# Kernel tuning notes

Measured on AMD Instinct MI355X. Metric: run time of the kernel, lower is better.

Reference implementation:

```python
import jax, jax.numpy as jnp
import numpy as np

B, T, N, F_IN = 8, 288, 2000, 1
E, ID, H, K = 128, 16, 128, 20
FL = T // 2 + 1  # rfft length = in_len//2 + 1
EPS_NORM = 1e-12
EPS_LN = 1e-8


def setup_inputs() -> dict:
    key = jax.random.key(0)
    k0, k1, k2, k3, k4 = jax.random.split(key, 5)
    return {
        "x": jax.random.normal(k0, (B, T, N, F_IN), jnp.float32),
        "Ex": jax.random.normal(k1, (FL, E), jnp.float32),
        "nodes": jax.random.normal(k2, (N, ID), jnp.float32),
        "Wd": jax.random.normal(k3, (N, E + ID, H), jnp.float32),
        "Wxabs": jax.random.normal(k4, (H, H), jnp.float32),
    }


def reference(x, Ex, nodes, Wd, Wxabs):
    # [B,T,N,F] -> take feature 0 -> [B,N,T]
    xt = jnp.transpose(x[:, :, :, 0], (0, 2, 1))
    xf = jnp.abs(jnp.fft.rfft(xt, axis=-1))  # [B,N,FL]
    # F.normalize p=2 over dim=1 (nodes), then dim=2 (freq): x / max(||x||, eps)
    xf = xf / jnp.clip(jnp.sqrt(jnp.sum(xf * xf, axis=1, keepdims=True)), EPS_NORM)
    xf = xf / jnp.clip(jnp.sqrt(jnp.sum(xf * xf, axis=2, keepdims=True)), EPS_NORM)
    xe = jnp.matmul(xf, Ex)  # [B,N,E]
    # cat(): append static node identity embedding per batch element
    xk = jnp.concatenate(
        [xe, jnp.broadcast_to(nodes, (xe.shape[0], N, ID))], axis=-1
    )  # [B,N,E+ID]
    # per-node weight bmm: [N,B,E+ID] @ [N,E+ID,H] -> [B,N,H]
    x1 = jax.nn.relu(jnp.einsum('bnd,ndh->bnh', xk, Wd))
    # LayerNorm over last two dims [N,H], eps=1e-8, no affine
    mu = jnp.mean(x1, axis=(1, 2), keepdims=True)
    var = jnp.mean((x1 - mu) ** 2, axis=(1, 2), keepdims=True)
    x2 = (x1 - mu) / jnp.sqrt(var + EPS_LN)
    # dropout is identity at inference
    adp = jnp.einsum('bnh,hk->bnk', x2, Wxabs)  # convt
    adj = jnp.einsum('bnh,bmh->bnm', adp, x1)  # [B,N,N]
    adp = jax.nn.relu(adj)
    # dy_mask_graph: per-row topk over dim=2 (torch dim=1 of the [N,N] slice),
    # binary mask via scatter of ones, then elementwise mask
    _, idx = jax.lax.top_k(adp, K)  # [B,N,K]
    bi = jnp.arange(adp.shape[0])[:, None, None]
    ni = jnp.arange(N)[None, :, None]
    mask = jnp.zeros_like(adp).at[bi, ni, idx].set(1.0)
    adj_masked = adp * mask
    return jax.nn.softmax(adj_masked, axis=2)
```

## Files before the change

kernel.cpp:

```cpp
#include <hip/hip_runtime.h>
#include <math.h>

#define BB 8
#define TT 288
#define NN 2000
#define FLEN 145
#define EE 128
#define IDD 16
#define HH 128
#define DKK 144
#define KTOP 20

typedef _Float16 half8 __attribute__((ext_vector_type(8)));
typedef float f32x4 __attribute__((ext_vector_type(4)));
typedef unsigned short ushort_t;

#define OFF_TW  ((size_t)0)
#define SZ_TW   ((size_t)TT*FLEN*2)
#define OFF_XF  (OFF_TW + SZ_TW)
#define SZ_XF   ((size_t)BB*FLEN*NN)
#define OFF_ICN (OFF_XF + SZ_XF)
#define OFF_IRN (OFF_ICN + (size_t)BB*FLEN)
#define OFF_XE  (OFF_IRN + (size_t)BB*NN)
#define SZ_BNH  ((size_t)BB*NN*HH)
#define OFF_X1  (OFF_XE + SZ_BNH)
#define OFF_ADP (OFF_X1 + SZ_BNH)
#define OFF_CSW (OFF_ADP + SZ_BNH)
#define OFF_LNS (OFF_CSW + HH)
#define OFF_LNF (OFF_LNS + 16)

__device__ __forceinline__ float wredSum(float v) {
#pragma unroll
  for (int o = 32; o > 0; o >>= 1) v += __shfl_down(v, o, 64);
  return v;
}
__device__ __forceinline__ float wredMax(float v) {
#pragma unroll
  for (int o = 32; o > 0; o >>= 1) v = fmaxf(v, __shfl_down(v, o, 64));
  return v;
}

__device__ __forceinline__ void split16(float v, ushort_t& hi, ushort_t& lo) {
  _Float16 h = (_Float16)v;
  _Float16 l = (_Float16)(v - (float)h);
  union { _Float16 f; ushort_t u; } a, b;
  a.f = h; b.f = l;
  hi = a.u; lo = b.u;
}

__global__ void k_init(const float* __restrict__ Wx, float* __restrict__ csw,
                       float* __restrict__ lns) {
  int k = threadIdx.x;
  float s = 0.f;
  for (int h = 0; h < HH; ++h) s += Wx[h * HH + k];
  csw[k] = s;
  if (k < 16) lns[k] = 0.f;
}

__global__ void k_tw(float* __restrict__ tw) {
  int id = blockIdx.x * 256 + threadIdx.x;
  if (id >= TT * FLEN) return;
  int t = id / FLEN, f = id % FLEN;
  int r = (t * f) % TT;
  double th = -2.0 * 3.14159265358979323846 * (double)r / (double)TT;
  tw[2 * id]     = (float)cos(th);
  tw[2 * id + 1] = (float)sin(th);
}

__global__ void k_dft(const float* __restrict__ x, const float* __restrict__ tw,
                      float* __restrict__ xf) {
  __shared__ __align__(16) float Xs[16][128];
  __shared__ __align__(16) float TWs[16][32][2];
  const int b = blockIdx.z;
  const int f0 = blockIdx.y * 32;
  const int n0 = blockIdx.x * 128;
  const int tid = threadIdx.x;
  const int tn = tid & 31;
  const int tf = tid >> 5;
  float ar[4][4] = {}, ai[4][4] = {};
  for (int t0 = 0; t0 < TT; t0 += 16) {
    __syncthreads();
    for (int l = tid; l < 512; l += 256) {
      int row = l >> 5, q = l & 31;
      int n = n0 + q * 4;
      const float* src = x + ((size_t)b * TT + (t0 + row)) * NN + n;
      float4 v = make_float4(0, 0, 0, 0);
      if (n + 3 < NN) v = *(const float4*)src;
      else {
        if (n + 0 < NN) v.x = src[0];
        if (n + 1 < NN) v.y = src[1];
        if (n + 2 < NN) v.z = src[2];
        if (n + 3 < NN) v.w = src[3];
      }
      *(float4*)&Xs[row][q * 4] = v;
    }
    for (int l = tid; l < 512; l += 256) {
      int row = l >> 5, ff = l & 31;
      int f = f0 + ff;
      float2 cs = make_float2(0, 0);
      if (f < FLEN) cs = *(const float2*)&tw[((size_t)(t0 + row) * FLEN + f) * 2];
      *(float2*)&TWs[row][ff][0] = cs;
    }
    __syncthreads();
#pragma unroll 4
    for (int t = 0; t < 16; ++t) {
      float4 xv = *(float4*)&Xs[t][tn * 4];
      float xx[4] = {xv.x, xv.y, xv.z, xv.w};
      float4 p0 = *(float4*)&TWs[t][tf * 4][0];
      float4 p1 = *(float4*)&TWs[t][tf * 4 + 2][0];
      float c[4] = {p0.x, p0.z, p1.x, p1.z};
      float s[4] = {p0.y, p0.w, p1.y, p1.w};
#pragma unroll
      for (int i = 0; i < 4; ++i)
#pragma unroll
        for (int j = 0; j < 4; ++j) {
          ar[i][j] = fmaf(xx[j], c[i], ar[i][j]);
          ai[i][j] = fmaf(xx[j], s[i], ai[i][j]);
        }
    }
  }
#pragma unroll
  for (int i = 0; i < 4; ++i) {
    int f = f0 + tf * 4 + i;
    if (f >= FLEN) continue;
    float* dst = &xf[((size_t)b * FLEN + f) * NN];
    float o[4];
#pragma unroll
    for (int j = 0; j < 4; ++j)
      o[j] = sqrtf(ar[i][j] * ar[i][j] + ai[i][j] * ai[i][j]);
    int n = n0 + tn * 4;
    if (n + 3 < NN) *(float4*)&dst[n] = make_float4(o[0], o[1], o[2], o[3]);
    else {
#pragma unroll
      for (int j = 0; j < 4; ++j) if (n + j < NN) dst[n + j] = o[j];
    }
  }
}

__global__ void k_colnorm(const float* __restrict__ xf, float* __restrict__ icn) {
  __shared__ float sc[4];
  int bf = blockIdx.x;
  const float* rowp = xf + (size_t)bf * NN;
  float s = 0.f;
  for (int i = threadIdx.x; i < NN; i += 256) { float v = rowp[i]; s = fmaf(v, v, s); }
  s = wredSum(s);
  int lane = threadIdx.x & 63, w = threadIdx.x >> 6;
  if (lane == 0) sc[w] = s;
  __syncthreads();
  if (threadIdx.x == 0)
    icn[bf] = 1.f / fmaxf(sqrtf(sc[0] + sc[1] + sc[2] + sc[3]), 1e-12f);
}

__global__ void k_rownorm(const float* __restrict__ xf, const float* __restrict__ icn,
                          float* __restrict__ irn) {
  int b = blockIdx.y;
  int n = blockIdx.x * 256 + threadIdx.x;
  if (n >= NN) return;
  float s = 0.f;
  for (int f = 0; f < FLEN; ++f) {
    float v = xf[((size_t)b * FLEN + f) * NN + n] * icn[b * FLEN + f];
    s = fmaf(v, v, s);
  }
  irn[b * NN + n] = 1.f / fmaxf(sqrtf(s), 1e-12f);
}

__global__ void k_xe(const float* __restrict__ xf, const float* __restrict__ icn,
                     const float* __restrict__ irn, const float* __restrict__ Ex,
                     float* __restrict__ xe) {
  __shared__ __align__(16) float As[16][64];
  __shared__ __align__(16) float Bs[16][128];
  const int b = blockIdx.y;
  const int n0 = blockIdx.x * 64;
  const int tid = threadIdx.x;
  const int tn = tid >> 4, te = tid & 15;
  float acc[4][8] = {};
  for (int f0 = 0; f0 < 160; f0 += 16) {
    __syncthreads();
    {
      int kt = tid >> 4, q = tid & 15;
      int f = f0 + kt;
      int n = n0 + q * 4;
      float4 v = make_float4(0, 0, 0, 0);
      if (f < FLEN) {
        float ic = icn[b * FLEN + f];
        const float* src = &xf[((size_t)b * FLEN + f) * NN + n];
        if (n + 3 < NN) v = *(const float4*)src;
        else {
          if (n + 0 < NN) v.x = src[0];
          if (n + 1 < NN) v.y = src[1];
          if (n + 2 < NN) v.z = src[2];
          if (n + 3 < NN) v.w = src[3];
        }
        v.x *= ic; v.y *= ic; v.z *= ic; v.w *= ic;
      }
      *(float4*)&As[kt][q * 4] = v;
    }
    for (int l = tid; l < 512; l += 256) {
      int kt = l >> 5, q = l & 31;
      int f = f0 + kt;
      float4 v = make_float4(0, 0, 0, 0);
      if (f < FLEN) v = *(const float4*)&Ex[(size_t)f * EE + q * 4];
      *(float4*)&Bs[kt][q * 4] = v;
    }
    __syncthreads();
#pragma unroll
    for (int k = 0; k < 16; ++k) {
      float4 a  = *(float4*)&As[k][tn * 4];
      float4 b0 = *(float4*)&Bs[k][te * 4];
      float4 b1 = *(float4*)&Bs[k][64 + te * 4];
      float av[4] = {a.x, a.y, a.z, a.w};
      float bv[8] = {b0.x, b0.y, b0.z, b0.w, b1.x, b1.y, b1.z, b1.w};
#pragma unroll
      for (int i = 0; i < 4; ++i)
#pragma unroll
        for (int j = 0; j < 8; ++j)
          acc[i][j] = fmaf(av[i], bv[j], acc[i][j]);
    }
  }
#pragma unroll
  for (int i = 0; i < 4; ++i) {
    int n = n0 + tn * 4 + i;
    if (n >= NN) continue;
    float sc = irn[b * NN + n];
    float* dst = &xe[((size_t)b * NN + n) * EE];
    *(float4*)&dst[te * 4] =
        make_float4(acc[i][0] * sc, acc[i][1] * sc, acc[i][2] * sc, acc[i][3] * sc);
    *(float4*)&dst[64 + te * 4] =
        make_float4(acc[i][4] * sc, acc[i][5] * sc, acc[i][6] * sc, acc[i][7] * sc);
  }
}

__global__ void k_x1(const float* xe, const float* __restrict__ nodes,
                     const float* __restrict__ Wd, float* __restrict__ x1,
                     ushort_t* x1hl) {
  __shared__ __align__(16) float xk[8][DKK];
  __shared__ float red[4][32][33];
  const int n = blockIdx.x;
  const int tid = threadIdx.x;
  {
    int b = tid >> 5, q = tid & 31;
    *(float4*)&xk[b][q * 4] = *(const float4*)&xe[((size_t)b * NN + n) * EE + q * 4];
  }
  if (tid < 128) {
    int b = tid >> 4, i = tid & 15;
    xk[b][EE + i] = nodes[(size_t)n * IDD + i];
  }
  __syncthreads();
  const int h4 = tid & 31;
  const int dg = tid >> 5;
  float acc[8][4] = {};
  for (int d = dg; d < DKK; d += 8) {
    float4 wv = *(const float4*)&Wd[((size_t)n * DKK + d) * HH + h4 * 4];
#pragma unroll
    for (int b = 0; b < 8; ++b) {
      float xv = xk[b][d];
      acc[b][0] = fmaf(xv, wv.x, acc[b][0]);
      acc[b][1] = fmaf(xv, wv.y, acc[b][1]);
      acc[b][2] = fmaf(xv, wv.z, acc[b][2]);
      acc[b][3] = fmaf(xv, wv.w, acc[b][3]);
    }
  }
#pragma unroll
  for (int b = 0; b < 8; ++b)
#pragma unroll
    for (int j = 0; j < 4; ++j)
      acc[b][j] += __shfl_xor(acc[b][j], 32, 64);
  const int wv_ = tid >> 6, lane = tid & 63;
  if (lane < 32) {
#pragma unroll
    for (int b = 0; b < 8; ++b)
#pragma unroll
      for (int j = 0; j < 4; ++j)
        red[wv_][lane][b * 4 + j] = acc[b][j];
  }
  __syncthreads();
#pragma unroll
  for (int o = 0; o < 4; ++o) {
    int idx = tid + o * 256;
    int b = idx >> 7, h = idx & 127;
    float s = red[0][h >> 2][b * 4 + (h & 3)] + red[1][h >> 2][b * 4 + (h & 3)] +
              red[2][h >> 2][b * 4 + (h & 3)] + red[3][h >> 2][b * 4 + (h & 3)];
    s = fmaxf(s, 0.f);
    x1[((size_t)b * NN + n) * HH + h] = s;
    ushort_t hi, lo;
    split16(s, hi, lo);
    size_t base = ((size_t)b * NN + n) * 256;
    x1hl[base + h] = hi;
    x1hl[base + 128 + h] = lo;
  }
}

__global__ void k_ln_stats(const float* __restrict__ x1, float* __restrict__ lns) {
  __shared__ float sc[4], sc2[4];
  int b = blockIdx.y, chunk = blockIdx.x;
  const float* base = x1 + (size_t)b * NN * HH + (size_t)chunk * 8000;
  float s = 0.f, s2 = 0.f;
  for (int i = threadIdx.x; i < 8000; i += 256) {
    float v = base[i];
    s += v; s2 = fmaf(v, v, s2);
  }
  s = wredSum(s); s2 = wredSum(s2);
  int lane = threadIdx.x & 63, w = threadIdx.x >> 6;
  if (lane == 0) { sc[w] = s; sc2[w] = s2; }
  __syncthreads();
  if (threadIdx.x == 0) {
    atomicAdd(&lns[b], sc[0] + sc[1] + sc[2] + sc[3]);
    atomicAdd(&lns[8 + b], sc2[0] + sc2[1] + sc2[2] + sc2[3]);
  }
}

__global__ void k_ln_final(const float* __restrict__ lns, float* __restrict__ lnf) {
  int b = threadIdx.x;
  if (b < 8) {
    float cnt = (float)(NN * HH);
    float mu = lns[b] / cnt;
    float var = fmaxf(lns[8 + b] / cnt - mu * mu, 0.f);
    lnf[b] = mu;
    lnf[8 + b] = 1.f / sqrtf(var + 1e-8f);
  }
}

__global__ void k_adp(const float* __restrict__ x1, const float* __restrict__ Wx,
                      const float* __restrict__ csw, const float* __restrict__ lnf,
                      ushort_t* __restrict__ adphl) {
  __shared__ __align__(16) float As[16][64];
  __shared__ __align__(16) float Bs[16][128];
  const int r0 = blockIdx.x * 64;
  const int tid = threadIdx.x;
  const int tn = tid >> 4, te = tid & 15;
  float acc[4][8] = {};
  for (int k0 = 0; k0 < HH; k0 += 16) {
    __syncthreads();
    {
      int rr = tid >> 2, kq = tid & 3;
      float4 v = *(const float4*)&x1[(size_t)(r0 + rr) * HH + k0 + kq * 4];
      As[kq * 4 + 0][rr] = v.x;
      As[kq * 4 + 1][rr] = v.y;
      As[kq * 4 + 2][rr] = v.z;
      As[kq * 4 + 3][rr] = v.w;
    }
    for (int l = tid; l < 512; l += 256) {
      int kt = l >> 5, q = l & 31;
      *(float4*)&Bs[kt][q * 4] = *(const float4*)&Wx[(size_t)(k0 + kt) * HH + q * 4];
    }
    __syncthreads();
#pragma unroll
    for (int k = 0; k < 16; ++k) {
      float4 a  = *(float4*)&As[k][tn * 4];
      float4 b0 = *(float4*)&Bs[k][te * 4];
      float4 b1 = *(float4*)&Bs[k][64 + te * 4];
      float av[4] = {a.x, a.y, a.z, a.w};
      float bv[8] = {b0.x, b0.y, b0.z, b0.w, b1.x, b1.y, b1.z, b1.w};
#pragma unroll
      for (int i = 0; i < 4; ++i)
#pragma unroll
        for (int j = 0; j < 8; ++j)
          acc[i][j] = fmaf(av[i], bv[j], acc[i][j]);
    }
  }
  float4 c0 = *(const float4*)&csw[te * 4];
  float4 c1 = *(const float4*)&csw[64 + te * 4];
  float cw[8] = {c0.x, c0.y, c0.z, c0.w, c1.x, c1.y, c1.z, c1.w};
#pragma unroll
  for (int i = 0; i < 4; ++i) {
    int r = r0 + tn * 4 + i;
    int b = r / NN;
    float mu = lnf[b], isd = lnf[8 + b];
    size_t base = (size_t)r * 256;
    ushort_t hi[8], lo[8];
#pragma unroll
    for (int j = 0; j < 8; ++j) {
      float o = (acc[i][j] - mu * cw[j]) * isd;
      split16(o, hi[j], lo[j]);
    }
    ushort4 u;
    u.x = hi[0]; u.y = hi[1]; u.z = hi[2]; u.w = hi[3];
    *(ushort4*)&adphl[base + te * 4] = u;
    u.x = hi[4]; u.y = hi[5]; u.z = hi[6]; u.w = hi[7];
    *(ushort4*)&adphl[base + 64 + te * 4] = u;
    u.x = lo[0]; u.y = lo[1]; u.z = lo[2]; u.w = lo[3];
    *(ushort4*)&adphl[base + 128 + te * 4] = u;
    u.x = lo[4]; u.y = lo[5]; u.z = lo[6]; u.w = lo[7];
    *(ushort4*)&adphl[base + 128 + 64 + te * 4] = u;
  }
}

__global__ void k_adj(const ushort_t* __restrict__ adphl,
                      const ushort_t* __restrict__ x1hl,
                      float* __restrict__ out) {
  __shared__ __align__(16) ushort_t lds[4][128 * 32];
  const int b = blockIdx.z;
  const int n0 = blockIdx.y * 128;
  const int m0 = blockIdx.x * 128;
  const int tid = threadIdx.x;
  const int w = tid >> 6;
  const int lane = tid & 63;
  const int quad = lane >> 4, r16 = lane & 15;
  const int rBase = (w >> 1) * 64;
  const int cBase = (w & 1) * 64;

  f32x4 acc[4][4];
#pragma unroll
  for (int i = 0; i < 4; ++i)
#pragma unroll
    for (int j = 0; j < 4; ++j)
      acc[i][j] = (f32x4){0.f, 0.f, 0.f, 0.f};

  const ushort_t* src = (w < 2) ? adphl : x1hl;
  const int rg0 = (w < 2) ? n0 : m0;
  const int loOff = (w & 1) ? 128 : 0;

  for (int k0 = 0; k0 < HH; k0 += 32) {
    __syncthreads();
#pragma unroll
    for (int i = 0; i < 8; ++i) {
      int cl = i * 64 + lane;
      int row = cl >> 2, c = cl & 3;
      int gr = rg0 + row; if (gr > NN - 1) gr = NN - 1;
      const uint4* gp =
          (const uint4*)(src + ((size_t)(b * NN + gr)) * 256 + loOff + k0 + c * 8);
      uint4 v = *gp;
      *(uint4*)&lds[w][row * 32 + ((c ^ (row & 3)) * 8)] = v;
    }
    __syncthreads();

    half8 Ah[4], Al[4], Bh[4], Bl[4];
#pragma unroll
    for (int i = 0; i < 4; ++i) {
      int ar = rBase + i * 16 + r16;
      int aoff = ar * 32 + ((quad ^ (ar & 3)) * 8);
      Ah[i] = *(half8*)&lds[0][aoff];
      Al[i] = *(half8*)&lds[1][aoff];
      int br = cBase + i * 16 + r16;
      int boff = br * 32 + ((quad ^ (br & 3)) * 8);
      Bh[i] = *(half8*)&lds[2][boff];
      Bl[i] = *(half8*)&lds[3][boff];
    }
#pragma unroll
    for (int i = 0; i < 4; ++i)
#pragma unroll
      for (int j = 0; j < 4; ++j) {
        acc[i][j] = __builtin_amdgcn_mfma_f32_16x16x32_f16(Ah[i], Bh[j], acc[i][j], 0, 0, 0);
        acc[i][j] = __builtin_amdgcn_mfma_f32_16x16x32_f16(Ah[i], Bl[j], acc[i][j], 0, 0, 0);
        acc[i][j] = __builtin_amdgcn_mfma_f32_16x16x32_f16(Al[i], Bh[j], acc[i][j], 0, 0, 0);
      }
  }

#pragma unroll
  for (int i = 0; i < 4; ++i) {
#pragma unroll
    for (int j = 0; j < 4; ++j) {
      int m = m0 + cBase + j * 16 + r16;
      if (m >= NN) continue;
#pragma unroll
      for (int reg = 0; reg < 4; ++reg) {
        int n = n0 + rBase + i * 16 + quad * 4 + reg;
        if (n >= NN) continue;
        out[((size_t)b * NN + n) * NN + m] = fmaxf(acc[i][j][reg], 0.f);
      }
    }
  }
}

__global__ void k_softmax(float* __restrict__ out) {
  __shared__ __align__(16) float row[NN];
  __shared__ float scr[4];
  __shared__ float swv[4];
  __shared__ int swi[4];
  __shared__ float tkv[KTOP];
  __shared__ int tki[KTOP];
  __shared__ float bcast[1];
  const int r = blockIdx.x;
  float* g = out + (size_t)r * NN;
  const int tid = threadIdx.x;
  const int lane = tid & 63, w = tid >> 6;
  for (int q = tid; q < 500; q += 256) *(float4*)&row[q * 4] = *(const float4*)&g[q * 4];
  __syncthreads();
  float m = 0.f;
  for (int i = tid; i < NN; i += 256) m = fmaxf(m, row[i]);
  m = wredMax(m);
  if (lane == 0) scr[w] = m;
  __syncthreads();
  m = fmaxf(fmaxf(scr[0], scr[1]), fmaxf(scr[2], scr[3]));
  const float thr = m - 87.f;
  float s = 0.f, c = 0.f;
  for (int i = tid; i < NN; i += 256) {
    float v = row[i];
    if (v > thr) { s += expf(v - m); c += 1.f; }
  }
  s = wredSum(s); c = wredSum(c);
  __syncthreads();
  if (lane == 0) scr[w] = s;
  __syncthreads();
  s = scr[0] + scr[1] + scr[2] + scr[3];
  __syncthreads();
  if (lane == 0) scr[w] = c;
  __syncthreads();
  c = scr[0] + scr[1] + scr[2] + scr[3];
  const float em = expf(-m);
  if (c <= 20.5f) {
    float D = s + ((float)NN - c) * em;
    float invD = 1.f / D;
    float defv = em * invD;
    for (int q = tid; q < 500; q += 256) {
      float4 v = *(float4*)&row[q * 4];
      float4 o;
      o.x = (v.x > thr) ? expf(v.x - m) * invD : defv;
      o.y = (v.y > thr) ? expf(v.y - m) * invD : defv;
      o.z = (v.z > thr) ? expf(v.z - m) * invD : defv;
      o.w = (v.w > thr) ? expf(v.w - m) * invD : defv;
      *(float4*)&g[q * 4] = o;
    }
  } else {
    for (int it = 0; it < KTOP; ++it) {
      float bv = -1.f; int bi = 0x7fffffff;
      for (int i = tid; i < NN; i += 256) {
        float v = row[i];
        if (v > bv) { bv = v; bi = i; }
      }
#pragma unroll
      for (int o = 32; o > 0; o >>= 1) {
        float ov = __shfl_down(bv, o, 64);
        int oi = __shfl_down(bi, o, 64);
        if (ov > bv || (ov == bv && oi < bi)) { bv = ov; bi = oi; }
      }
      __syncthreads();
      if (lane == 0) { swv[w] = bv; swi[w] = bi; }
      __syncthreads();
      if (tid == 0) {
        float fv = swv[0]; int fi = swi[0];
        for (int ww = 1; ww < 4; ++ww)
          if (swv[ww] > fv || (swv[ww] == fv && swi[ww] < fi)) { fv = swv[ww]; fi = swi[ww]; }
        tkv[it] = fv; tki[it] = fi;
        row[fi] = -1.f;
      }
      __syncthreads();
    }
    if (tid == 0) {
      float D = ((float)(NN - KTOP)) * em;
      for (int it = 0; it < KTOP; ++it) D += expf(tkv[it] - m);
      bcast[0] = 1.f / D;
    }
    __syncthreads();
    float invD = bcast[0];
    float defv = em * invD;
    for (int q = tid; q < 500; q += 256)
      *(float4*)&g[q * 4] = make_float4(defv, defv, defv, defv);
    __syncthreads();
    if (tid < KTOP) g[tki[tid]] = expf(tkv[tid] - m) * invD;
  }
}

extern "C" void kernel_launch(void* const* d_in, const int* in_sizes, int n_in,
                              void* d_out, int out_size, void* d_ws, size_t ws_size,
                              hipStream_t stream) {
  const float* x     = (const float*)d_in[0];
  const float* Ex    = (const float*)d_in[1];
  const float* nodes = (const float*)d_in[2];
  const float* Wd    = (const float*)d_in[3];
  const float* Wx    = (const float*)d_in[4];
  float* out = (float*)d_out;
  float* w = (float*)d_ws;
  float* tw  = w + OFF_TW;
  float* xf  = w + OFF_XF;
  float* icn = w + OFF_ICN;
  float* irn = w + OFF_IRN;
  float* xe  = w + OFF_XE;
  float* x1  = w + OFF_X1;
  float* csw = w + OFF_CSW;
  float* lns = w + OFF_LNS;
  float* lnf = w + OFF_LNF;
  ushort_t* adphl = (ushort_t*)(w + OFF_ADP);
  ushort_t* x1hl  = (ushort_t*)(w + OFF_XE);

  k_init<<<1, 128, 0, stream>>>(Wx, csw, lns);
  k_tw<<<(TT * FLEN + 255) / 256, 256, 0, stream>>>(tw);
  k_dft<<<dim3(16, 5, BB), 256, 0, stream>>>(x, tw, xf);
  k_colnorm<<<BB * FLEN, 256, 0, stream>>>(xf, icn);
  k_rownorm<<<dim3(8, BB), 256, 0, stream>>>(xf, icn, irn);
  k_xe<<<dim3(32, BB), 256, 0, stream>>>(xf, icn, irn, Ex, xe);
  k_x1<<<NN, 256, 0, stream>>>(xe, nodes, Wd, x1, x1hl);
  k_ln_stats<<<dim3(32, BB), 256, 0, stream>>>(x1, lns);
  k_ln_final<<<1, 64, 0, stream>>>(lns, lnf);
  k_adp<<<250, 256, 0, stream>>>(x1, Wx, csw, lnf, adphl);
  k_adj<<<dim3(16, 16, BB), 256, 0, stream>>>(adphl, x1hl, out);
  k_softmax<<<BB * NN, 256, 0, stream>>>(out);
}
```

Before: 488.9 us.

## Fuse adjacency GEMM with top-k masked softmax using LDS row cache

After: 582.2 us. +19.1%, slower.

```diff
diff --git a/kernel.cpp b/kernel.cpp
--- a/kernel.cpp
+++ b/kernel.cpp
@@ -29,6 +29,9 @@
 #define OFF_LNS (OFF_CSW + HH)
 #define OFF_LNF (OFF_LNS + 16)
 
+#define CACHE_W 2064
+#define FUSED_LDS_BYTES ((16 * CACHE_W + 2 * 8 * 64) * 4)
+
 __device__ __forceinline__ float wredSum(float v) {
 #pragma unroll
   for (int o = 32; o > 0; o >>= 1) v += __shfl_down(v, o, 64);
@@ -37,6 +40,16 @@
 __device__ __forceinline__ float wredMax(float v) {
 #pragma unroll
   for (int o = 32; o > 0; o >>= 1) v = fmaxf(v, __shfl_down(v, o, 64));
+  return v;
+}
+__device__ __forceinline__ float wredSumAll(float v) {
+#pragma unroll
+  for (int o = 32; o > 0; o >>= 1) v += __shfl_xor(v, o, 64);
+  return v;
+}
+__device__ __forceinline__ float wredMaxAll(float v) {
+#pragma unroll
+  for (int o = 32; o > 0; o >>= 1) v = fmaxf(v, __shfl_xor(v, o, 64));
   return v;
 }
 
@@ -385,169 +398,177 @@
   }
 }
 
-__global__ void k_adj(const ushort_t* __restrict__ adphl,
-                      const ushort_t* __restrict__ x1hl,
-                      float* __restrict__ out) {
-  __shared__ __align__(16) ushort_t lds[4][128 * 32];
-  const int b = blockIdx.z;
-  const int n0 = blockIdx.y * 128;
-  const int m0 = blockIdx.x * 128;
+__global__ __launch_bounds__(512, 1) void k_fused(
+    const ushort_t* __restrict__ adphl, const ushort_t* __restrict__ x1hl,
+    float* __restrict__ out) {
+  extern __shared__ float smem[];
+  float* cache = smem;
+  float* scrV = smem + 16 * CACHE_W;
+  int*   scrI = (int*)(scrV + 8 * 64);
+
+  const int b = blockIdx.y;
+  const int n0 = blockIdx.x * 16;
   const int tid = threadIdx.x;
   const int w = tid >> 6;
   const int lane = tid & 63;
   const int quad = lane >> 4, r16 = lane & 15;
-  const int rBase = (w >> 1) * 64;
-  const int cBase = (w & 1) * 64;
-
-  f32x4 acc[4][4];
-#pragma unroll
-  for (int i = 0; i < 4; ++i)
-#pragma unroll
-    for (int j = 0; j < 4; ++j)
-      acc[i][j] = (f32x4){0.f, 0.f, 0.f, 0.f};
-
-  const ushort_t* src = (w < 2) ? adphl : x1hl;
-  const int rg0 = (w < 2) ? n0 : m0;
-  const int loOff = (w & 1) ? 128 : 0;
-
-  for (int k0 = 0; k0 < HH; k0 += 32) {
-    __syncthreads();
-#pragma unroll
-    for (int i = 0; i < 8; ++i) {
-      int cl = i * 64 + lane;
-      int row = cl >> 2, c = cl & 3;
-      int gr = rg0 + row; if (gr > NN - 1) gr = NN - 1;
-      const uint4* gp =
-          (const uint4*)(src + ((size_t)(b * NN + gr)) * 256 + loOff + k0 + c * 8);
-      uint4 v = *gp;
-      *(uint4*)&lds[w][row * 32 + ((c ^ (row & 3)) * 8)] = v;
-    }
-    __syncthreads();
-
-    half8 Ah[4], Al[4], Bh[4], Bl[4];
+
+  half8 Ah[4], Al[4];
+  {
+    const ushort_t* abase =
+        adphl + ((size_t)(b * NN + n0 + r16)) * 256 + quad * 8;
+#pragma unroll
+    for (int ks = 0; ks < 4; ++ks) {
+      Ah[ks] = *(const half8*)(abase + ks * 32);
+      Al[ks] = *(const half8*)(abase + 128 + ks * 32);
+    }
+  }
+  for (int s = 0; s < 4; ++s) {
+    const int mb = s * 512 + w * 64;
 #pragma unroll
     for (int i = 0; i < 4; ++i) {
-      int ar = rBase + i * 16 + r16;
-      int aoff = ar * 32 + ((quad ^ (ar & 3)) * 8);
-      Ah[i] = *(half8*)&lds[0][aoff];
-      Al[i] = *(half8*)&lds[1][aoff];
-      int br = cBase + i * 16 + r16;
-      int boff = br * 32 + ((quad ^ (br & 3)) * 8);
-      Bh[i] = *(half8*)&lds[2][boff];
-      Bl[i] = *(half8*)&lds[3][boff];
-    }
-#pragma unroll
-    for (int i = 0; i < 4; ++i)
-#pragma unroll
-      for (int j = 0; j < 4; ++j) {
-        acc[i][j] = __builtin_amdgcn_mfma_f32_16x16x32_f16(Ah[i], Bh[j], acc[i][j], 0, 0, 0);
-        acc[i][j] = __builtin_amdgcn_mfma_f32_16x16x32_f16(Ah[i], Bl[j], acc[i][j], 0, 0, 0);
-        acc[i][j] = __builtin_amdgcn_mfma_f32_16x16x32_f16(Al[i], Bh[j], acc[i][j], 0, 0, 0);
-      }
-  }
-
-#pragma unroll
-  for (int i = 0; i < 4; ++i) {
-#pragma unroll
-    for (int j = 0; j < 4; ++j) {
-      int m = m0 + cBase + j * 16 + r16;
-      if (m >= NN) continue;
+      const int mt = mb + i * 16 + r16;
+      const int mc = (mt < NN) ? mt : NN - 1;
+      const ushort_t* bbase =
+          x1hl + ((size_t)(b * NN + mc)) * 256 + quad * 8;
+      half8 Bh[4], Bl[4];
+#pragma unroll
+      for (int ks = 0; ks < 4; ++ks) {
+        Bh[ks] = *(const half8*)(bbase + ks * 32);
+        Bl[ks] = *(const half8*)(bbase + 128 + ks * 32);
+      }
+      f32x4 acc = (f32x4){0.f, 0.f, 0.f, 0.f};
+#pragma unroll
+      for (int ks = 0; ks < 4; ++ks) {
+        acc = __builtin_amdgcn_mfma_f32_16x16x32_f16(Ah[ks], Bh[ks], acc, 0, 0, 0);
+        acc = __builtin_amdgcn_mfma_f32_16x16x32_f16(Ah[ks], Bl[ks], acc, 0, 0, 0);
+        acc = __builtin_amdgcn_mfma_f32_16x16x32_f16(Al[ks], Bh[ks], acc, 0, 0, 0);
+      }
 #pragma unroll
       for (int reg = 0; reg < 4; ++reg) {
-        int n = n0 + rBase + i * 16 + quad * 4 + reg;
-        if (n >= NN) continue;
-        out[((size_t)b * NN + n) * NN + m] = fmaxf(acc[i][j][reg], 0.f);
-      }
-    }
-  }
-}
-
-__global__ void k_softmax(float* __restrict__ out) {
-  __shared__ __align__(16) float row[NN];
-  __shared__ float scr[4];
-  __shared__ float swv[4];
-  __shared__ int swi[4];
-  __shared__ float tkv[KTOP];
-  __shared__ int tki[KTOP];
-  __shared__ float bcast[1];
-  const int r = blockIdx.x;
-  float* g = out + (size_t)r * NN;
-  const int tid = threadIdx.x;
-  const int lane = tid & 63, w = tid >> 6;
-  for (int q = tid; q < 500; q += 256) *(float4*)&row[q * 4] = *(const float4*)&g[q * 4];
+        int row = quad * 4 + reg;
+        float v = (mt < NN) ? fmaxf(acc[reg], 0.f) : -1.f;
+        cache[row * CACHE_W + mt] = v;
+      }
+    }
+  }
   __syncthreads();
-  float m = 0.f;
-  for (int i = tid; i < NN; i += 256) m = fmaxf(m, row[i]);
-  m = wredMax(m);
-  if (lane == 0) scr[w] = m;
-  __syncthreads();
-  m = fmaxf(fmaxf(scr[0], scr[1]), fmaxf(scr[2], scr[3]));
-  const float thr = m - 87.f;
-  float s = 0.f, c = 0.f;
-  for (int i = tid; i < NN; i += 256) {
-    float v = row[i];
-    if (v > thr) { s += expf(v - m); c += 1.f; }
-  }
-  s = wredSum(s); c = wredSum(c);
-  __syncthreads();
-  if (lane == 0) scr[w] = s;
-  __syncthreads();
-  s = scr[0] + scr[1] + scr[2] + scr[3];
-  __syncthreads();
-  if (lane == 0) scr[w] = c;
-  __syncthreads();
-  c = scr[0] + scr[1] + scr[2] + scr[3];
-  const float em = expf(-m);
-  if (c <= 20.5f) {
-    float D = s + ((float)NN - c) * em;
-    float invD = 1.f / D;
-    float defv = em * invD;
-    for (int q = tid; q < 500; q += 256) {
-      float4 v = *(float4*)&row[q * 4];
-      float4 o;
-      o.x = (v.x > thr) ? expf(v.x - m) * invD : defv;
-      o.y = (v.y > thr) ? expf(v.y - m) * invD : defv;
-      o.z = (v.z > thr) ? expf(v.z - m) * invD : defv;
-      o.w = (v.w > thr) ? expf(v.w - m) * invD : defv;
-      *(float4*)&g[q * 4] = o;
-    }
-  } else {
-    for (int it = 0; it < KTOP; ++it) {
-      float bv = -1.f; int bi = 0x7fffffff;
-      for (int i = tid; i < NN; i += 256) {
-        float v = row[i];
-        if (v > bv) { bv = v; bi = i; }
-      }
-#pragma unroll
-      for (int o = 32; o > 0; o >>= 1) {
-        float ov = __shfl_down(bv, o, 64);
-        int oi = __shfl_down(bi, o, 64);
-        if (ov > bv || (ov == bv && oi < bi)) { bv = ov; bi = oi; }
-      }
-      __syncthreads();
-      if (lane == 0) { swv[w] = bv; swi[w] = bi; }
-      __syncthreads();
-      if (tid == 0) {
-        float fv = swv[0]; int fi = swi[0];
-        for (int ww = 1; ww < 4; ++ww)
-          if (swv[ww] > fv || (swv[ww] == fv && swi[ww] < fi)) { fv = swv[ww]; fi = swi[ww]; }
-        tkv[it] = fv; tki[it] = fi;
-        row[fi] = -1.f;
-      }
-      __syncthreads();
-    }
-    if (tid == 0) {
-      float D = ((float)(NN - KTOP)) * em;
-      for (int it = 0; it < KTOP; ++it) D += expf(tkv[it] - m);
-      bcast[0] = 1.f / D;
-    }
-    __syncthreads();
-    float invD = bcast[0];
-    float defv = em * invD;
-    for (int q = tid; q < 500; q += 256)
-      *(float4*)&g[q * 4] = make_float4(defv, defv, defv, defv);
-    __syncthreads();
-    if (tid < KTOP) g[tki[tid]] = expf(tkv[tid] - m) * invD;
+
+  for (int rr = 0; rr < 2; ++rr) {
+    const int row = w * 2 + rr;
+    const float* crow = cache + row * CACHE_W;
+    f32x4 V[8];
+#pragma unroll
+    for (int j = 0; j < 8; ++j)
+      V[j] = *(const f32x4*)&crow[j * 256 + lane * 4];
+
+    float mx = -1.f, cp = 0.f;
+#pragma unroll
+    for (int j = 0; j < 8; ++j)
+#pragma unroll
+      for (int e = 0; e < 4; ++e) {
+        mx = fmaxf(mx, V[j][e]);
+        cp += (V[j][e] > 0.f) ? 1.f : 0.f;
+      }
+    const float m = wredMaxAll(mx);
+    const float cpos = wredSumAll(cp);
+    const float em = expf(-m);
+    float* g = out + ((size_t)(b * NN + n0 + row)) * NN;
+
+    if (cpos <= 20.5f) {
+      float s = 0.f;
+#pragma unroll
+      for (int j = 0; j < 8; ++j)
+#pragma unroll
+        for (int e = 0; e < 4; ++e)
+          if (V[j][e] > 0.f) s += expf(V[j][e] - m);
+      s = wredSumAll(s);
+      const float invD = 1.f / (s + (2000.f - cpos) * em);
+      const float defv = em * invD;
+#pragma unroll
+      for (int j = 0; j < 8; ++j) {
+        int m0 = j * 256 + lane * 4;
+        if (m0 >= NN) continue;
+        float4 o;
+        o.x = (V[j][0] > 0.f) ? expf(V[j][0] - m) * invD : defv;
+        o.y = (V[j][1] > 0.f) ? expf(V[j][1] - m) * invD : defv;
+        o.z = (V[j][2] > 0.f) ? expf(V[j][2] - m) * invD : defv;
+        o.w = (V[j][3] > 0.f) ? expf(V[j][3] - m) * invD : defv;
+        *(float4*)&g[m0] = o;
+      }
+    } else {
+      float tval = 0.f, cf = cpos;
+      if (cpos > 64.5f) {
+        float tlo = 0.f, thi = m;
+        bool found = false;
+        for (int it = 0; it < 64 && !found; ++it) {
+          float mid = (it < 12)
+              ? 0.5f * (tlo + thi)
+              : __uint_as_float((__float_as_uint(tlo) + __float_as_uint(thi)) >> 1);
+          float c = 0.f;
+#pragma unroll
+          for (int j = 0; j < 8; ++j)
+#pragma unroll
+            for (int e = 0; e < 4; ++e)
+              c += (V[j][e] > mid) ? 1.f : 0.f;
+          c = wredSumAll(c);
+          if (c > 64.5f) tlo = mid;
+          else if (c < 19.5f) thi = mid;
+          else { tval = mid; cf = c; found = true; }
+        }
+        if (!found) { tval = tlo; cf = 64.f; }
+      }
+      int cI = (int)(cf + 0.5f);
+      if (cI > 64) cI = 64;
+
+      float* sv = scrV + w * 64;
+      int* si = scrI + w * 64;
+      int base = 0;
+#pragma unroll
+      for (int j = 0; j < 8; ++j)
+#pragma unroll
+        for (int e = 0; e < 4; ++e) {
+          bool p = V[j][e] > tval;
+          unsigned long long msk = __ballot(p);
+          if (p) {
+            int pos = base + (int)__popcll(msk & ((1ull << lane) - 1ull));
+            if (pos < 64) { sv[pos] = V[j][e]; si[pos] = j * 256 + lane * 4 + e; }
+          }
+          base += (int)__popcll(msk);
+        }
+      asm volatile("s_waitcnt lgkmcnt(0)" ::: "memory");
+
+      float cv = (lane < cI) ? sv[lane] : -1.f;
+      int ci = (lane < cI) ? si[lane] : 0x7fffffff;
+#pragma unroll
+      for (int k = 2; k <= 64; k <<= 1)
+#pragma unroll
+        for (int j = k >> 1; j > 0; j >>= 1) {
+          float ov = __shfl_xor(cv, j, 64);
+          int oi = __shfl_xor(ci, j, 64);
+          bool otherBetter = (ov > cv) || (ov == cv && oi < ci);
+          bool iAmLow = (lane & j) == 0;
+          bool desc = (lane & k) == 0;
+          bool take = (desc == iAmLow) ? otherBetter : !otherBetter;
+          if (take) { cv = ov; ci = oi; }
+        }
+      const float t20 = __shfl(cv, 19, 64);
+      float e20 = (lane < 20) ? expf(cv - m) : 0.f;
+      const float s20 = wredSumAll(e20);
+      const float invD = 1.f / (s20 + (2000.f - 20.f) * em);
+      const float defv = em * invD;
+#pragma unroll
+      for (int j = 0; j < 8; ++j) {
+        int m0 = j * 256 + lane * 4;
+        if (m0 >= NN) continue;
+        float4 o;
+        o.x = (V[j][0] >= t20) ? expf(V[j][0] - m) * invD : defv;
+        o.y = (V[j][1] >= t20) ? expf(V[j][1] - m) * invD : defv;
+        o.z = (V[j][2] >= t20) ? expf(V[j][2] - m) * invD : defv;
+        o.w = (V[j][3] >= t20) ? expf(V[j][3] - m) * invD : defv;
+        *(float4*)&g[m0] = o;
+      }
+    }
   }
 }
 
@@ -573,6 +594,14 @@
   ushort_t* adphl = (ushort_t*)(w + OFF_ADP);
   ushort_t* x1hl  = (ushort_t*)(w + OFF_XE);
 
+  static int _once = []() {
+    (void)hipFuncSetAttribute((const void*)k_fused,
+                              hipFuncAttributeMaxDynamicSharedMemorySize,
+                              FUSED_LDS_BYTES);
+    return 0;
+  }();
+  (void)_once;
+
   k_init<<<1, 128, 0, stream>>>(Wx, csw, lns);
   k_tw<<<(TT * FLEN + 255) / 256, 256, 0, stream>>>(tw);
   k_dft<<<dim3(16, 5, BB), 256, 0, stream>>>(x, tw, xf);
@@ -583,6 +612,5 @@
   k_ln_stats<<<dim3(32, BB), 256, 0, stream>>>(x1, lns);
   k_ln_final<<<1, 64, 0, stream>>>(lns, lnf);
   k_adp<<<250, 256, 0, stream>>>(x1, Wx, csw, lnf, adphl);
-  k_adj<<<dim3(16, 16, BB), 256, 0, stream>>>(adphl, x1hl, out);
-  k_softmax<<<BB * NN, 256, 0, stream>>>(out);
-}
+  k_fused<<<dim3(125, BB), 512, FUSED_LDS_BYTES, stream>>>(adphl, x1hl, out);
+}
```
